# Kernel tuning notes

Hardware: AMD Instinct MI355X
Metric: run time of the kernel (lower is better)

## Reference

```python
import jax, jax.numpy as jnp
import numpy as np


def setup_inputs() -> dict:
    key = jax.random.key(0)
    kx, kw, kt, ks, kd, km = jax.random.split(key, 6)
    B, N, E, H, D = 1, 100000, 3200000, 8, 64
    X = jax.random.normal(kx, (B, N, H, D), dtype=jnp.float32)
    # glorot_uniform-like init for [D, H, 1]
    limit = (6.0 / (D + H)) ** 0.5
    attn_kernel = jax.random.uniform(kw, (D, H, 1), dtype=jnp.float32, minval=-limit, maxval=limit)
    targets = jax.random.randint(kt, (B, E), 0, N)
    sources = jax.random.randint(ks, (B, E), 0, N)
    degree = jax.random.uniform(kd, (B, N), dtype=jnp.float32)
    # tf.nn.dropout(x, 0.5): keep w.p. 0.5, scale kept by 1/0.5 = 2
    drop_mask = (jax.random.uniform(km, (B, E, H)) < 0.5).astype(jnp.float32) * 2.0
    return {"X": X, "attn_kernel": attn_kernel, "targets": targets,
            "sources": sources, "degree": degree, "drop_mask": drop_mask, "N": N}


def reference(X, attn_kernel, targets, sources, degree, drop_mask, N):
    # X: [B, N, H, D]; attn_kernel: [D, H, 1]; targets/sources: [B, E]
    B, _, H, D = X.shape
    E = targets.shape[1]
    W = attn_kernel[:, :, 0]                          # [D, H]
    attn = jnp.einsum('bnhd,dh->bnh', X, W)           # per-node scalar per head
    # gather to edges (tf.gather batch_dims=1): [B, E, H]
    e = jnp.take_along_axis(attn, sources[..., None], axis=1)
    e = jnp.tanh(e)
    # TF unsorted_segment_max with rank-2 ids pools over (batch, edge) jointly
    ids = targets.reshape(B * E)
    ef = e.reshape(B * E, H)
    m = jax.ops.segment_max(ef, ids, num_segments=N)  # [N, H]
    ef = jnp.exp(ef - m[ids])
    s = jax.ops.segment_max(ef, ids, num_segments=N) + 1e-9  # NOTE: max, not sum (faithful)
    ef = ef / s[ids]
    out = ef.reshape(B, E, H) * drop_mask
    return out[..., None]                             # [B, E, H, 1]
```

## Files before the change

kernel.cpp:

```cpp
#include <hip/hip_runtime.h>
#include <stdint.h>

#define HD 8
#define DD 64

__device__ __forceinline__ unsigned fmap(float f) {
    unsigned u = __float_as_uint(f);
    return u ^ (unsigned)(((int)u >> 31) | 0x80000000);
}
__device__ __forceinline__ float funmap(unsigned u) {
    u ^= ((int)u < 0) ? 0x80000000u : 0xFFFFFFFFu;
    return __uint_as_float(u);
}
#define FMAP_NEG_INF 0x007FFFFFu

__global__ __launch_bounds__(256) void attn_tanh_kernel(
    const float* __restrict__ X, const float* __restrict__ Wk,
    float* __restrict__ t, unsigned* __restrict__ m_u, int N)
{
    __shared__ float Ws[DD * HD];
    int tid = threadIdx.x;
    for (int i = tid; i < DD * HD; i += 256) Ws[i] = Wk[i];
    __syncthreads();

    int wave = tid >> 6, lane = tid & 63;
    int node = blockIdx.x * 4 + wave;
    if (node >= N) return;

    const float4* X4 = (const float4*)X + (size_t)node * 128;
    float p0, p1;
    {
        int idx = lane;
        float4 xv = X4[idx];
        int h = idx >> 4, d0 = (idx & 15) << 2;
        p0 = xv.x * Ws[(d0 + 0) * HD + h] + xv.y * Ws[(d0 + 1) * HD + h]
           + xv.z * Ws[(d0 + 2) * HD + h] + xv.w * Ws[(d0 + 3) * HD + h];
    }
    {
        int idx = 64 + lane;
        float4 xv = X4[idx];
        int h = idx >> 4, d0 = (idx & 15) << 2;
        p1 = xv.x * Ws[(d0 + 0) * HD + h] + xv.y * Ws[(d0 + 1) * HD + h]
           + xv.z * Ws[(d0 + 2) * HD + h] + xv.w * Ws[(d0 + 3) * HD + h];
    }
    for (int off = 8; off; off >>= 1) {
        p0 += __shfl_xor(p0, off);
        p1 += __shfl_xor(p1, off);
    }
    if ((lane & 15) == 0) {
        int g = lane >> 4;
        size_t base = (size_t)node * HD;
        t[base + g]      = tanhf(p0);
        t[base + 4 + g]  = tanhf(p1);
        m_u[base + g]     = FMAP_NEG_INF;
        m_u[base + 4 + g] = FMAP_NEG_INF;
    }
}

__global__ __launch_bounds__(256) void seg_max_kernel(
    const int* __restrict__ sources, const int* __restrict__ targets,
    const float* __restrict__ t, unsigned* __restrict__ m_u, int E)
{
    int e = blockIdx.x * 256 + threadIdx.x;
    if (e >= E) return;
    int s  = sources[e];
    int tg = targets[e];
    const float4* t4 = (const float4*)t;
    float4 a = t4[(size_t)s * 2];
    float4 b = t4[(size_t)s * 2 + 1];
    unsigned* mp = m_u + (size_t)tg * HD;
    const uint4* m4 = (const uint4*)mp;
    uint4 c0 = m4[0];
    uint4 c1 = m4[1];
    unsigned f;
    f = fmap(a.x); if (f > c0.x) atomicMax(mp + 0, f);
    f = fmap(a.y); if (f > c0.y) atomicMax(mp + 1, f);
    f = fmap(a.z); if (f > c0.z) atomicMax(mp + 2, f);
    f = fmap(a.w); if (f > c0.w) atomicMax(mp + 3, f);
    f = fmap(b.x); if (f > c1.x) atomicMax(mp + 4, f);
    f = fmap(b.y); if (f > c1.y) atomicMax(mp + 5, f);
    f = fmap(b.z); if (f > c1.z) atomicMax(mp + 6, f);
    f = fmap(b.w); if (f > c1.w) atomicMax(mp + 7, f);
}

__global__ __launch_bounds__(256) void finalize_kernel(
    const int* __restrict__ sources, const int* __restrict__ targets,
    const float* __restrict__ t, const unsigned* __restrict__ m_u,
    const float* __restrict__ dm, float* __restrict__ out, int E)
{
    int e = blockIdx.x * 256 + threadIdx.x;
    if (e >= E) return;
    int s  = sources[e];
    int tg = targets[e];
    const float4* t4 = (const float4*)t;
    float4 a = t4[(size_t)s * 2];
    float4 b = t4[(size_t)s * 2 + 1];
    const uint4* m4 = (const uint4*)m_u;
    uint4 mu0 = m4[(size_t)tg * 2];
    uint4 mu1 = m4[(size_t)tg * 2 + 1];
    const float4* dm4 = (const float4*)dm;
    float4 d0 = dm4[(size_t)e * 2];
    float4 d1 = dm4[(size_t)e * 2 + 1];
    float4 o0, o1;
    o0.x = expf(a.x - funmap(mu0.x)) * d0.x;
    o0.y = expf(a.y - funmap(mu0.y)) * d0.y;
    o0.z = expf(a.z - funmap(mu0.z)) * d0.z;
    o0.w = expf(a.w - funmap(mu0.w)) * d0.w;
    o1.x = expf(b.x - funmap(mu1.x)) * d1.x;
    o1.y = expf(b.y - funmap(mu1.y)) * d1.y;
    o1.z = expf(b.z - funmap(mu1.z)) * d1.z;
    o1.w = expf(b.w - funmap(mu1.w)) * d1.w;
    float4* out4 = (float4*)out;
    out4[(size_t)e * 2]     = o0;
    out4[(size_t)e * 2 + 1] = o1;
}

extern "C" void kernel_launch(void* const* d_in, const int* in_sizes, int n_in,
                              void* d_out, int out_size, void* d_ws, size_t ws_size,
                              hipStream_t stream)
{
    const float* X       = (const float*)d_in[0];
    const float* Wk      = (const float*)d_in[1];
    const int*   targets = (const int*)d_in[2];
    const int*   sources = (const int*)d_in[3];
    const float* dm      = (const float*)d_in[5];

    int E = in_sizes[2];
    int N = in_sizes[4];

    float*    t   = (float*)d_ws;
    unsigned* m_u = (unsigned*)d_ws + (size_t)N * HD;

    float* out = (float*)d_out;

    int blocksA = (N + 3) / 4;
    attn_tanh_kernel<<<blocksA, 256, 0, stream>>>(X, Wk, t, m_u, N);

    int blocksE = (E + 255) / 256;
    seg_max_kernel<<<blocksE, 256, 0, stream>>>(sources, targets, t, m_u, E);
    finalize_kernel<<<blocksE, 256, 0, stream>>>(sources, targets, t, m_u, dm, out, E);
}
```

Measured before the change: 661.5 us.

## Store per-node tanh scores and segment maxima as packed bf16 for edge gathers

The per-node tanh attention scores are stored as packed bf16 pairs, 16 bytes per node instead of 32. A new pack_m kernel converts the segment maxima to the same packed bf16 layout, so both random per-edge gathers read half as many bytes. Streaming index, dropout-mask and output accesses now use nontemporal loads and stores, and the projection kernel handles two nodes per wave. The cost is an extra kernel launch and bf16 rounding of the scores, which adds small errors to the exp outputs.

```diff
diff --git a/kernel.cpp b/kernel.cpp
--- a/kernel.cpp
+++ b/kernel.cpp
@@ -3,6 +3,9 @@
 
 #define HD 8
 #define DD 64
+
+typedef float  vf4 __attribute__((ext_vector_type(4)));
+typedef unsigned vu4 __attribute__((ext_vector_type(4)));
 
 __device__ __forceinline__ unsigned fmap(float f) {
     unsigned u = __float_as_uint(f);
@@ -14,9 +17,17 @@
 }
 #define FMAP_NEG_INF 0x007FFFFFu
 
+__device__ __forceinline__ unsigned pack_bf16_rne(float a, float b) {
+    unsigned ua = __float_as_uint(a); ua += 0x7FFF + ((ua >> 16) & 1);
+    unsigned ub = __float_as_uint(b); ub += 0x7FFF + ((ub >> 16) & 1);
+    return (ua >> 16) | (ub & 0xFFFF0000u);
+}
+__device__ __forceinline__ float bf_lo(unsigned u) { return __uint_as_float(u << 16); }
+__device__ __forceinline__ float bf_hi(unsigned u) { return __uint_as_float(u & 0xFFFF0000u); }
+
 __global__ __launch_bounds__(256) void attn_tanh_kernel(
     const float* __restrict__ X, const float* __restrict__ Wk,
-    float* __restrict__ t, unsigned* __restrict__ m_u, int N)
+    unsigned* __restrict__ t_pk, uint2* __restrict__ m_init, int N)
 {
     __shared__ float Ws[DD * HD];
     int tid = threadIdx.x;
@@ -24,95 +35,112 @@
     __syncthreads();
 
     int wave = tid >> 6, lane = tid & 63;
-    int node = blockIdx.x * 4 + wave;
-    if (node >= N) return;
+    int n0 = (blockIdx.x * 4 + wave) * 2;
+    if (n0 >= N) return;
+    bool two = (n0 + 1 < N);
 
-    const float4* X4 = (const float4*)X + (size_t)node * 128;
-    float p0, p1;
-    {
-        int idx = lane;
-        float4 xv = X4[idx];
-        int h = idx >> 4, d0 = (idx & 15) << 2;
-        p0 = xv.x * Ws[(d0 + 0) * HD + h] + xv.y * Ws[(d0 + 1) * HD + h]
-           + xv.z * Ws[(d0 + 2) * HD + h] + xv.w * Ws[(d0 + 3) * HD + h];
-    }
-    {
-        int idx = 64 + lane;
-        float4 xv = X4[idx];
-        int h = idx >> 4, d0 = (idx & 15) << 2;
-        p1 = xv.x * Ws[(d0 + 0) * HD + h] + xv.y * Ws[(d0 + 1) * HD + h]
-           + xv.z * Ws[(d0 + 2) * HD + h] + xv.w * Ws[(d0 + 3) * HD + h];
-    }
+    const vf4* Xa = (const vf4*)X + (size_t)n0 * 128;
+    vf4 z = {0.f, 0.f, 0.f, 0.f};
+    vf4 xv0 = __builtin_nontemporal_load(Xa + lane);
+    vf4 xv1 = __builtin_nontemporal_load(Xa + 64 + lane);
+    vf4 xv2 = two ? __builtin_nontemporal_load(Xa + 128 + lane) : z;
+    vf4 xv3 = two ? __builtin_nontemporal_load(Xa + 192 + lane) : z;
+
+    int h0 = lane >> 4, d0 = (lane & 15) << 2;
+    int h1 = 4 + h0;
+    float w00 = Ws[(d0 + 0) * HD + h0], w01 = Ws[(d0 + 1) * HD + h0],
+          w02 = Ws[(d0 + 2) * HD + h0], w03 = Ws[(d0 + 3) * HD + h0];
+    float w10 = Ws[(d0 + 0) * HD + h1], w11 = Ws[(d0 + 1) * HD + h1],
+          w12 = Ws[(d0 + 2) * HD + h1], w13 = Ws[(d0 + 3) * HD + h1];
+
+    float p0 = xv0.x * w00 + xv0.y * w01 + xv0.z * w02 + xv0.w * w03;
+    float p1 = xv1.x * w10 + xv1.y * w11 + xv1.z * w12 + xv1.w * w13;
+    float p2 = xv2.x * w00 + xv2.y * w01 + xv2.z * w02 + xv2.w * w03;
+    float p3 = xv3.x * w10 + xv3.y * w11 + xv3.z * w12 + xv3.w * w13;
+
     for (int off = 8; off; off >>= 1) {
         p0 += __shfl_xor(p0, off);
         p1 += __shfl_xor(p1, off);
+        p2 += __shfl_xor(p2, off);
+        p3 += __shfl_xor(p3, off);
     }
     if ((lane & 15) == 0) {
         int g = lane >> 4;
-        size_t base = (size_t)node * HD;
-        t[base + g]      = tanhf(p0);
-        t[base + 4 + g]  = tanhf(p1);
-        m_u[base + g]     = FMAP_NEG_INF;
-        m_u[base + 4 + g] = FMAP_NEG_INF;
+        t_pk[(size_t)n0 * 4 + g] = pack_bf16_rne(tanhf(p0), tanhf(p1));
+        m_init[(size_t)n0 * 4 + g] = make_uint2(FMAP_NEG_INF, FMAP_NEG_INF);
+        if (two) {
+            t_pk[(size_t)(n0 + 1) * 4 + g] = pack_bf16_rne(tanhf(p2), tanhf(p3));
+            m_init[(size_t)(n0 + 1) * 4 + g] = make_uint2(FMAP_NEG_INF, FMAP_NEG_INF);
+        }
     }
 }
 
 __global__ __launch_bounds__(256) void seg_max_kernel(
     const int* __restrict__ sources, const int* __restrict__ targets,
-    const float* __restrict__ t, unsigned* __restrict__ m_u, int E)
+    const uint4* __restrict__ t_pk4, unsigned* __restrict__ m_u, int E)
 {
     int e = blockIdx.x * 256 + threadIdx.x;
     if (e >= E) return;
-    int s  = sources[e];
-    int tg = targets[e];
-    const float4* t4 = (const float4*)t;
-    float4 a = t4[(size_t)s * 2];
-    float4 b = t4[(size_t)s * 2 + 1];
+    int s  = __builtin_nontemporal_load(sources + e);
+    int tg = __builtin_nontemporal_load(targets + e);
+    uint4 tv = t_pk4[s];
     unsigned* mp = m_u + (size_t)tg * HD;
     const uint4* m4 = (const uint4*)mp;
     uint4 c0 = m4[0];
     uint4 c1 = m4[1];
     unsigned f;
-    f = fmap(a.x); if (f > c0.x) atomicMax(mp + 0, f);
-    f = fmap(a.y); if (f > c0.y) atomicMax(mp + 1, f);
-    f = fmap(a.z); if (f > c0.z) atomicMax(mp + 2, f);
-    f = fmap(a.w); if (f > c0.w) atomicMax(mp + 3, f);
-    f = fmap(b.x); if (f > c1.x) atomicMax(mp + 4, f);
-    f = fmap(b.y); if (f > c1.y) atomicMax(mp + 5, f);
-    f = fmap(b.z); if (f > c1.z) atomicMax(mp + 6, f);
-    f = fmap(b.w); if (f > c1.w) atomicMax(mp + 7, f);
+    f = fmap(bf_lo(tv.x)); if (f > c0.x) atomicMax(mp + 0, f);
+    f = fmap(bf_hi(tv.x)); if (f > c0.y) atomicMax(mp + 1, f);
+    f = fmap(bf_lo(tv.y)); if (f > c0.z) atomicMax(mp + 2, f);
+    f = fmap(bf_hi(tv.y)); if (f > c0.w) atomicMax(mp + 3, f);
+    f = fmap(bf_lo(tv.z)); if (f > c1.x) atomicMax(mp + 4, f);
+    f = fmap(bf_hi(tv.z)); if (f > c1.y) atomicMax(mp + 5, f);
+    f = fmap(bf_lo(tv.w)); if (f > c1.z) atomicMax(mp + 6, f);
+    f = fmap(bf_hi(tv.w)); if (f > c1.w) atomicMax(mp + 7, f);
+}
+
+__global__ __launch_bounds__(256) void pack_m_kernel(
+    const unsigned* __restrict__ m_u, uint4* __restrict__ m_pk, int N)
+{
+    int n = blockIdx.x * 256 + threadIdx.x;
+    if (n >= N) return;
+    const uint4* mu4 = (const uint4*)m_u + (size_t)n * 2;
+    uint4 c0 = mu4[0];
+    uint4 c1 = mu4[1];
+    uint4 o;
+    o.x = (__float_as_uint(funmap(c0.x)) >> 16) | (__float_as_uint(funmap(c0.y)) & 0xFFFF0000u);
+    o.y = (__float_as_uint(funmap(c0.z)) >> 16) | (__float_as_uint(funmap(c0.w)) & 0xFFFF0000u);
+    o.z = (__float_as_uint(funmap(c1.x)) >> 16) | (__float_as_uint(funmap(c1.y)) & 0xFFFF0000u);
+    o.w = (__float_as_uint(funmap(c1.z)) >> 16) | (__float_as_uint(funmap(c1.w)) & 0xFFFF0000u);
+    m_pk[n] = o;
 }
 
 __global__ __launch_bounds__(256) void finalize_kernel(
     const int* __restrict__ sources, const int* __restrict__ targets,
-    const float* __restrict__ t, const unsigned* __restrict__ m_u,
+    const uint4* __restrict__ t_pk4, const uint4* __restrict__ m_pk,
     const float* __restrict__ dm, float* __restrict__ out, int E)
 {
     int e = blockIdx.x * 256 + threadIdx.x;
     if (e >= E) return;
-    int s  = sources[e];
-    int tg = targets[e];
-    const float4* t4 = (const float4*)t;
-    float4 a = t4[(size_t)s * 2];
-    float4 b = t4[(size_t)s * 2 + 1];
-    const uint4* m4 = (const uint4*)m_u;
-    uint4 mu0 = m4[(size_t)tg * 2];
-    uint4 mu1 = m4[(size_t)tg * 2 + 1];
-    const float4* dm4 = (const float4*)dm;
-    float4 d0 = dm4[(size_t)e * 2];
-    float4 d1 = dm4[(size_t)e * 2 + 1];
-    float4 o0, o1;
-    o0.x = expf(a.x - funmap(mu0.x)) * d0.x;
-    o0.y = expf(a.y - funmap(mu0.y)) * d0.y;
-    o0.z = expf(a.z - funmap(mu0.z)) * d0.z;
-    o0.w = expf(a.w - funmap(mu0.w)) * d0.w;
-    o1.x = expf(b.x - funmap(mu1.x)) * d1.x;
-    o1.y = expf(b.y - funmap(mu1.y)) * d1.y;
-    o1.z = expf(b.z - funmap(mu1.z)) * d1.z;
-    o1.w = expf(b.w - funmap(mu1.w)) * d1.w;
-    float4* out4 = (float4*)out;
-    out4[(size_t)e * 2]     = o0;
-    out4[(size_t)e * 2 + 1] = o1;
+    int s  = __builtin_nontemporal_load(sources + e);
+    int tg = __builtin_nontemporal_load(targets + e);
+    uint4 tv = t_pk4[s];
+    uint4 mv = m_pk[tg];
+    const vf4* dm4 = (const vf4*)dm;
+    vf4 d0 = __builtin_nontemporal_load(dm4 + (size_t)e * 2);
+    vf4 d1 = __builtin_nontemporal_load(dm4 + (size_t)e * 2 + 1);
+    vf4 o0, o1;
+    o0.x = expf(bf_lo(tv.x) - bf_lo(mv.x)) * d0.x;
+    o0.y = expf(bf_lo(tv.y) - bf_lo(mv.y)) * d0.y;
+    o0.z = expf(bf_lo(tv.z) - bf_lo(mv.z)) * d0.z;
+    o0.w = expf(bf_lo(tv.w) - bf_lo(mv.w)) * d0.w;
+    o1.x = expf(bf_hi(tv.x) - bf_hi(mv.x)) * d1.x;
+    o1.y = expf(bf_hi(tv.y) - bf_hi(mv.y)) * d1.y;
+    o1.z = expf(bf_hi(tv.z) - bf_hi(mv.z)) * d1.z;
+    o1.w = expf(bf_hi(tv.w) - bf_hi(mv.w)) * d1.w;
+    vf4* out4 = (vf4*)out;
+    __builtin_nontemporal_store(o0, out4 + (size_t)e * 2);
+    __builtin_nontemporal_store(o1, out4 + (size_t)e * 2 + 1);
 }
 
 extern "C" void kernel_launch(void* const* d_in, const int* in_sizes, int n_in,
@@ -128,15 +156,20 @@
     int E = in_sizes[2];
     int N = in_sizes[4];
 
-    float*    t   = (float*)d_ws;
-    unsigned* m_u = (unsigned*)d_ws + (size_t)N * HD;
+    unsigned* t_pk = (unsigned*)d_ws;
+    unsigned* m_u  = (unsigned*)d_ws + (size_t)N * 4;
+    uint4*    m_pk = (uint4*)((unsigned*)d_ws + (size_t)N * 12);
 
     float* out = (float*)d_out;
 
-    int blocksA = (N + 3) / 4;
-    attn_tanh_kernel<<<blocksA, 256, 0, stream>>>(X, Wk, t, m_u, N);
+    int blocksA = (N + 7) / 8;
+    attn_tanh_kernel<<<blocksA, 256, 0, stream>>>(X, Wk, t_pk, (uint2*)m_u, N);
 
     int blocksE = (E + 255) / 256;
-    seg_max_kernel<<<blocksE, 256, 0, stream>>>(sources, targets, t, m_u, E);
-    finalize_kernel<<<blocksE, 256, 0, stream>>>(sources, targets, t, m_u, dm, out, E);
+    seg_max_kernel<<<blocksE, 256, 0, stream>>>(sources, targets, (const uint4*)t_pk, m_u, E);
+
+    int blocksN = (N + 255) / 256;
+    pack_m_kernel<<<blocksN, 256, 0, stream>>>(m_u, m_pk, N);
+
+    finalize_kernel<<<blocksE, 256, 0, stream>>>(sources, targets, (const uint4*)t_pk, m_pk, dm, out, E);
 }
```

New measurement: 639.9 us. 3.3% less time.
